# Kernel optimization log

Measured on AMD Instinct MI355X. Metric: run time of the kernel, lower is better.

Reference implementation:

```python
import jax, jax.numpy as jnp
import numpy as np

B, T, IN, CELL, OUT = 512, 32, 512, 128, 128


def setup_inputs() -> dict:
    key = jax.random.key(0)
    ks = jax.random.split(key, 6)
    d = IN + CELL
    w = lambda k, shape, fan: jax.random.normal(k, shape, jnp.float32) / np.sqrt(fan).astype(np.float32)
    return {
        "x": jax.random.normal(ks[0], (B, T, IN), jnp.float32),
        "Wf": w(ks[1], (d, CELL), d), "bf": jnp.zeros((CELL,), jnp.float32),
        "Wi1": w(ks[2], (d, CELL), d), "bi1": jnp.zeros((CELL,), jnp.float32),
        "Wi2": w(ks[3], (d, CELL), d), "bi2": jnp.zeros((CELL,), jnp.float32),
        "Wo": w(ks[4], (d, CELL), d), "bo": jnp.zeros((CELL,), jnp.float32),
        "Wc": w(ks[5], (CELL, OUT), CELL), "bc": jnp.zeros((OUT,), jnp.float32),
    }


def reference(x, Wf, bf, Wi1, bi1, Wi2, bi2, Wo, bo, Wc, bc):
    # Faithful to MyLSTM.forward: loop runs x.shape[1] times; each iteration
    # concatenates the FULL [B,T,CELL] cell_state with the FULL [B,T,IN] x
    # (x is never sliced per step). Only the last iteration's output matters,
    # but we carry it through the scan to match the loop structure exactly.
    Tn = x.shape[1]
    c0 = jnp.zeros(x.shape[:2] + (Wf.shape[1],), x.dtype)
    out0 = jnp.zeros(x.shape[:2] + (Wc.shape[1],), x.dtype)

    def step(carry, _):
        c, _prev_out = carry
        inp = jnp.concatenate([c, x], axis=-1)  # [B,T,CELL+IN]
        f = jax.nn.sigmoid(inp @ Wf + bf)
        c = c * f + jax.nn.sigmoid(inp @ Wi1 + bi1) * jnp.tanh(inp @ Wi2 + bi2)
        o = jax.nn.sigmoid(inp @ Wo + bo) * jnp.tanh(c)
        out = jax.nn.softmax(o @ Wc + bc, axis=2)  # out_features != 1 branch
        return (c, out), None

    (c, out), _ = jax.lax.scan(step, (c0, out0), None, length=Tn)
    return out, c
```

## Files before the change

kernel.cpp:

```cpp
#include <hip/hip_runtime.h>
#include <stdint.h>

#define ROWS  16384
#define CELL  128
#define INF   512
#define RPB   32
#define NSTEP 32

#define LOG2E 1.4426950408889634f

typedef _Float16 f16x8 __attribute__((ext_vector_type(8)));
typedef _Float16 f16x4 __attribute__((ext_vector_type(4)));
typedef float    f32x16 __attribute__((ext_vector_type(16)));

#define MFMA32(a, b, c) __builtin_amdgcn_mfma_f32_32x32x16_f16((a), (b), (c), 0, 0, 0)

#if __has_builtin(__builtin_amdgcn_exp2f)
#define EXP2(x) __builtin_amdgcn_exp2f(x)
#else
#define EXP2(x) __expf((x) * 0.6931471805599453f)
#endif
#define RCP(x) __builtin_amdgcn_rcpf(x)

#define XOFF  65536
#define WCOFF 327680
#define WSTOT 344064

__device__ __forceinline__ unsigned short f2h_bits(float f) {
  _Float16 h = (_Float16)f;
  return *(unsigned short*)&h;
}

__global__ __launch_bounds__(256) void prep_kernel(
    const float* __restrict__ Wf, const float* __restrict__ Wi1,
    const float* __restrict__ Wi2, const float* __restrict__ Wo,
    const float* __restrict__ Wc, unsigned short* __restrict__ ws) {
  int id = blockIdx.x * blockDim.x + threadIdx.x;
  if (id >= WSTOT) return;
  const float* Wg[4] = {Wf, Wi1, Wi2, Wo};
  const float sc[4] = {-LOG2E, -LOG2E, 2.f * LOG2E, -LOG2E};
  if (id < XOFF) {
    int g = id >> 14, r = id & 16383;
    int w = r >> 12, ks = (r >> 9) & 7, lane = (r >> 3) & 63, j = r & 7;
    int k = ks * 16 + ((lane >> 5) << 3) + j;
    int n = w * 32 + (lane & 31);
    ws[id] = f2h_bits(Wg[g][k * CELL + n] * sc[g]);
  } else if (id < WCOFF) {
    int t = id - XOFF;
    int g = t >> 16, r = t & 65535;
    int w = r >> 14, ks = (r >> 9) & 31, lane = (r >> 3) & 63, j = r & 7;
    int k = ks * 16 + ((lane >> 5) << 3) + j;
    int n = w * 32 + (lane & 31);
    ws[id] = f2h_bits(Wg[g][(CELL + k) * CELL + n] * sc[g]);
  } else {
    int r = id - WCOFF;
    int w = r >> 12, ks = (r >> 9) & 7, lane = (r >> 3) & 63, j = r & 7;
    int k = ks * 16 + ((lane >> 5) << 3) + j;
    int n = w * 32 + (lane & 31);
    ws[id] = f2h_bits(Wc[k * CELL + n] * LOG2E);
  }
}

__global__ __launch_bounds__(256, 2) void lstm_kernel(
    const float* __restrict__ x,
    const float* __restrict__ bf_, const float* __restrict__ bi1,
    const float* __restrict__ bi2, const float* __restrict__ bo,
    const float* __restrict__ bc,
    const unsigned short* __restrict__ ws, float* __restrict__ out) {

  __shared__ union {
    _Float16 xs[32][264];
    struct {
      _Float16 o[32][136];
      float    s[32][132];
    } ep;
  } uS;
  __shared__ _Float16 cT[2][32][136];

  const int tid  = threadIdx.x;
  const int lane = tid & 63;
  const int w    = tid >> 6;
  const int n31  = lane & 31;
  const int l5   = lane >> 5;
  const int r0   = blockIdx.x * RPB;

  const _Float16* Aw  = (const _Float16*)ws;
  const _Float16* Xw  = (const _Float16*)ws + XOFF;
  const _Float16* Wcw = (const _Float16*)ws + WCOFF;

  f32x16 u[4];
#pragma unroll
  for (int g = 0; g < 4; ++g)
#pragma unroll
    for (int i = 0; i < 16; ++i) u[g][i] = 0.f;

  const float* xbase = x + (size_t)r0 * INF;
#pragma unroll 1
  for (int ch = 0; ch < 2; ++ch) {
    if (ch) __syncthreads();
#pragma unroll
    for (int i = 0; i < 8; ++i) {
      int flat = tid + i * 256;
      int row = flat >> 6, c4 = flat & 63;
      const float4 v = ((const float4*)(xbase + (size_t)row * INF + ch * 256))[c4];
      f16x4 h = {(_Float16)v.x, (_Float16)v.y, (_Float16)v.z, (_Float16)v.w};
      *(f16x4*)&uS.xs[row][c4 * 4] = h;
    }
    __syncthreads();
#pragma unroll 2
    for (int ksl = 0; ksl < 16; ++ksl) {
      f16x8 b = *(const f16x8*)&uS.xs[n31][ksl * 16 + l5 * 8];
      int ks = ch * 16 + ksl;
#pragma unroll
      for (int g = 0; g < 4; ++g) {
        f16x8 a = *(const f16x8*)(Xw + (((g * 4 + w) * 32 + ks) * 64 + lane) * 8);
        u[g] = MFMA32(a, b, u[g]);
      }
    }
  }
#pragma unroll
  for (int reg = 0; reg < 16; ++reg) {
    int col = w * 32 + (reg & 3) + 8 * (reg >> 2) + 4 * l5;
    u[0][reg] += bf_[col] * (-LOG2E);
    u[1][reg] += bi1[col] * (-LOG2E);
    u[2][reg] += bi2[col] * (2.f * LOG2E);
    u[3][reg] += bo[col]  * (-LOG2E);
  }

  f16x8 wr[3][8];
#pragma unroll
  for (int g = 0; g < 3; ++g)
#pragma unroll
    for (int ks = 0; ks < 8; ++ks)
      wr[g][ks] = *(const f16x8*)(Aw + (((g * 4 + w) * 8 + ks) * 64 + lane) * 8);

  f32x16 cr;
#pragma unroll
  for (int reg = 0; reg < 16; ++reg) {
    float ig = RCP(1.f + EXP2(u[1][reg]));
    float gg = fmaf(-2.f, RCP(1.f + EXP2(u[2][reg])), 1.f);
    cr[reg] = ig * gg;
  }
#pragma unroll
  for (int qd = 0; qd < 4; ++qd) {
    f16x4 p = {(_Float16)cr[qd * 4 + 0], (_Float16)cr[qd * 4 + 1],
               (_Float16)cr[qd * 4 + 2], (_Float16)cr[qd * 4 + 3]};
    *(f16x4*)&cT[0][n31][w * 32 + qd * 8 + l5 * 4] = p;
  }
  __syncthreads();

#pragma unroll 1
  for (int t = 1; t < NSTEP - 1; ++t) {
    const int rb = (t + 1) & 1, wb = t & 1;
    f16x8 b[8];
#pragma unroll
    for (int ks = 0; ks < 8; ++ks)
      b[ks] = *(const f16x8*)&cT[rb][n31][ks * 16 + l5 * 8];
    f32x16 zf = u[0], zi1 = u[1], zi2 = u[2];
#pragma unroll
    for (int ks = 0; ks < 8; ++ks) {
      zf  = MFMA32(wr[0][ks], b[ks], zf);
      zi1 = MFMA32(wr[1][ks], b[ks], zi1);
      zi2 = MFMA32(wr[2][ks], b[ks], zi2);
    }
#pragma unroll
    for (int reg = 0; reg < 16; ++reg) {
      float fg = RCP(1.f + EXP2(zf[reg]));
      float ig = RCP(1.f + EXP2(zi1[reg]));
      float gg = fmaf(-2.f, RCP(1.f + EXP2(zi2[reg])), 1.f);
      cr[reg] = fmaf(cr[reg], fg, ig * gg);
    }
#pragma unroll
    for (int qd = 0; qd < 4; ++qd) {
      f16x4 p = {(_Float16)cr[qd * 4 + 0], (_Float16)cr[qd * 4 + 1],
                 (_Float16)cr[qd * 4 + 2], (_Float16)cr[qd * 4 + 3]};
      *(f16x4*)&cT[wb][n31][w * 32 + qd * 8 + l5 * 4] = p;
    }
    __syncthreads();
  }

  {
    f16x8 b[8];
#pragma unroll
    for (int ks = 0; ks < 8; ++ks)
      b[ks] = *(const f16x8*)&cT[0][n31][ks * 16 + l5 * 8];
    f32x16 zf = u[0], zi1 = u[1], zi2 = u[2], zo = u[3];
#pragma unroll
    for (int ks = 0; ks < 8; ++ks) {
      f16x8 wof = *(const f16x8*)(Aw + (((3 * 4 + w) * 8 + ks) * 64 + lane) * 8);
      zf  = MFMA32(wr[0][ks], b[ks], zf);
      zi1 = MFMA32(wr[1][ks], b[ks], zi1);
      zi2 = MFMA32(wr[2][ks], b[ks], zi2);
      zo  = MFMA32(wof, b[ks], zo);
    }
    float ovv[16];
#pragma unroll
    for (int reg = 0; reg < 16; ++reg) {
      float fg = RCP(1.f + EXP2(zf[reg]));
      float ig = RCP(1.f + EXP2(zi1[reg]));
      float gg = fmaf(-2.f, RCP(1.f + EXP2(zi2[reg])), 1.f);
      float cn = fmaf(cr[reg], fg, ig * gg);
      cr[reg] = cn;
      float th = fmaf(-2.f, RCP(1.f + EXP2(cn * (2.f * LOG2E))), 1.f);
      ovv[reg] = RCP(1.f + EXP2(zo[reg])) * th;
    }
#pragma unroll
    for (int qd = 0; qd < 4; ++qd) {
      f16x4 p = {(_Float16)ovv[qd * 4 + 0], (_Float16)ovv[qd * 4 + 1],
                 (_Float16)ovv[qd * 4 + 2], (_Float16)ovv[qd * 4 + 3]};
      *(f16x4*)&uS.ep.o[n31][w * 32 + qd * 8 + l5 * 4] = p;
    }
    __syncthreads();
  }

  {
    f32x16 sa;
#pragma unroll
    for (int i = 0; i < 16; ++i) sa[i] = 0.f;
#pragma unroll
    for (int ks = 0; ks < 8; ++ks) {
      f16x8 a = *(const f16x8*)(Wcw + ((w * 8 + ks) * 64 + lane) * 8);
      f16x8 b = *(const f16x8*)&uS.ep.o[n31][ks * 16 + l5 * 8];
      sa = MFMA32(a, b, sa);
    }
#pragma unroll
    for (int reg = 0; reg < 16; ++reg) {
      int col = w * 32 + (reg & 3) + 8 * (reg >> 2) + 4 * l5;
      sa[reg] += bc[col] * LOG2E;
    }
#pragma unroll
    for (int qd = 0; qd < 4; ++qd) {
      float4 p = {sa[qd * 4 + 0], sa[qd * 4 + 1], sa[qd * 4 + 2], sa[qd * 4 + 3]};
      *(float4*)&uS.ep.s[n31][w * 32 + qd * 8 + l5 * 4] = p;
    }
    __syncthreads();

#pragma unroll
    for (int rr = 0; rr < 8; ++rr) {
      int r = w * 8 + rr;
      float v0 = uS.ep.s[r][lane];
      float v1 = uS.ep.s[r][lane + 64];
      float m = fmaxf(v0, v1);
#pragma unroll
      for (int off = 32; off; off >>= 1) m = fmaxf(m, __shfl_xor(m, off, 64));
      float e0 = EXP2(v0 - m), e1 = EXP2(v1 - m);
      float sm = e0 + e1;
#pragma unroll
      for (int off = 32; off; off >>= 1) sm += __shfl_xor(sm, off, 64);
      float inv = RCP(sm);
      size_t base = (size_t)(r0 + r) * 128;
      out[base + lane]      = e0 * inv;
      out[base + lane + 64] = e1 * inv;
    }

#pragma unroll
    for (int qd = 0; qd < 4; ++qd) {
      float4 p = {cr[qd * 4 + 0], cr[qd * 4 + 1], cr[qd * 4 + 2], cr[qd * 4 + 3]};
      *(float4*)&out[(size_t)ROWS * 128 + (size_t)(r0 + n31) * 128 +
                     w * 32 + qd * 8 + l5 * 4] = p;
    }
  }
}

extern "C" void kernel_launch(void* const* d_in, const int* in_sizes, int n_in,
                              void* d_out, int out_size, void* d_ws, size_t ws_size,
                              hipStream_t stream) {
  const float* x   = (const float*)d_in[0];
  const float* Wf  = (const float*)d_in[1];
  const float* bf_ = (const float*)d_in[2];
  const float* Wi1 = (const float*)d_in[3];
  const float* bi1 = (const float*)d_in[4];
  const float* Wi2 = (const float*)d_in[5];
  const float* bi2 = (const float*)d_in[6];
  const float* Wo  = (const float*)d_in[7];
  const float* bo  = (const float*)d_in[8];
  const float* Wc  = (const float*)d_in[9];
  const float* bc  = (const float*)d_in[10];
  unsigned short* ws = (unsigned short*)d_ws;
  float* out = (float*)d_out;

  hipLaunchKernelGGL(prep_kernel, dim3((WSTOT + 255) / 256), dim3(256), 0, stream,
                     Wf, Wi1, Wi2, Wo, Wc, ws);
  hipLaunchKernelGGL(lstm_kernel, dim3(ROWS / RPB), dim3(256), 0, stream,
                     x, bf_, bi1, bi2, bo, bc, ws, out);
}
```

Before: 178.9 us.

## Process 64 rows per block with two MFMA row groups and swizzled cell LDS

Each block now handles 64 rows as two 32-row groups, so every wave's register-resident recurrent weights feed twice as many MFMAs and the per-step barrier cost is spread over more work. The output-gate input projection moves to shared memory to free registers. The cell-state LDS layout becomes an XOR-swizzled buffer to avoid bank conflicts. In exchange, occupancy drops to one block per CU, the grid is halved (256 blocks), and register pressure rises with the doubled accumulators.

```diff
diff --git a/kernel.cpp b/kernel.cpp
--- a/kernel.cpp
+++ b/kernel.cpp
@@ -4,7 +4,7 @@
 #define ROWS  16384
 #define CELL  128
 #define INF   512
-#define RPB   32
+#define RPB   64
 #define NSTEP 32
 
 #define LOG2E 1.4426950408889634f
@@ -61,7 +61,7 @@
   }
 }
 
-__global__ __launch_bounds__(256, 2) void lstm_kernel(
+__global__ __launch_bounds__(256, 1) void lstm_kernel(
     const float* __restrict__ x,
     const float* __restrict__ bf_, const float* __restrict__ bi1,
     const float* __restrict__ bi2, const float* __restrict__ bo,
@@ -69,37 +69,41 @@
     const unsigned short* __restrict__ ws, float* __restrict__ out) {
 
   __shared__ union {
-    _Float16 xs[32][264];
+    _Float16 xs[64][268];
     struct {
-      _Float16 o[32][136];
-      float    s[32][132];
+      _Float16 o[64][136];
+      float    s[64][132];
     } ep;
   } uS;
-  __shared__ _Float16 cT[2][32][136];
+  __shared__ _Float16 cT[2][2][32][128];
+  __shared__ float    uo[2][128][33];
 
   const int tid  = threadIdx.x;
   const int lane = tid & 63;
   const int w    = tid >> 6;
   const int n31  = lane & 31;
   const int l5   = lane >> 5;
+  const int key  = (n31 & 15) << 1;
   const int r0   = blockIdx.x * RPB;
 
   const _Float16* Aw  = (const _Float16*)ws;
   const _Float16* Xw  = (const _Float16*)ws + XOFF;
   const _Float16* Wcw = (const _Float16*)ws + WCOFF;
 
-  f32x16 u[4];
+  f32x16 u[4][2];
 #pragma unroll
   for (int g = 0; g < 4; ++g)
 #pragma unroll
-    for (int i = 0; i < 16; ++i) u[g][i] = 0.f;
+    for (int gr = 0; gr < 2; ++gr)
+#pragma unroll
+      for (int i = 0; i < 16; ++i) u[g][gr][i] = 0.f;
 
   const float* xbase = x + (size_t)r0 * INF;
 #pragma unroll 1
   for (int ch = 0; ch < 2; ++ch) {
     if (ch) __syncthreads();
 #pragma unroll
-    for (int i = 0; i < 8; ++i) {
+    for (int i = 0; i < 16; ++i) {
       int flat = tid + i * 256;
       int row = flat >> 6, c4 = flat & 63;
       const float4 v = ((const float4*)(xbase + (size_t)row * INF + ch * 256))[c4];
@@ -109,22 +113,29 @@
     __syncthreads();
 #pragma unroll 2
     for (int ksl = 0; ksl < 16; ++ksl) {
-      f16x8 b = *(const f16x8*)&uS.xs[n31][ksl * 16 + l5 * 8];
+      f16x8 b0 = *(const f16x8*)&uS.xs[n31][ksl * 16 + l5 * 8];
+      f16x8 b1 = *(const f16x8*)&uS.xs[32 + n31][ksl * 16 + l5 * 8];
       int ks = ch * 16 + ksl;
 #pragma unroll
       for (int g = 0; g < 4; ++g) {
         f16x8 a = *(const f16x8*)(Xw + (((g * 4 + w) * 32 + ks) * 64 + lane) * 8);
-        u[g] = MFMA32(a, b, u[g]);
+        u[g][0] = MFMA32(a, b0, u[g][0]);
+        u[g][1] = MFMA32(a, b1, u[g][1]);
       }
     }
   }
 #pragma unroll
   for (int reg = 0; reg < 16; ++reg) {
     int col = w * 32 + (reg & 3) + 8 * (reg >> 2) + 4 * l5;
-    u[0][reg] += bf_[col] * (-LOG2E);
-    u[1][reg] += bi1[col] * (-LOG2E);
-    u[2][reg] += bi2[col] * (2.f * LOG2E);
-    u[3][reg] += bo[col]  * (-LOG2E);
+    float b0v = bf_[col] * (-LOG2E);
+    float b1v = bi1[col] * (-LOG2E);
+    float b2v = bi2[col] * (2.f * LOG2E);
+    float b3v = bo[col]  * (-LOG2E);
+    u[0][0][reg] += b0v; u[0][1][reg] += b0v;
+    u[1][0][reg] += b1v; u[1][1][reg] += b1v;
+    u[2][0][reg] += b2v; u[2][1][reg] += b2v;
+    uo[0][col][n31] = u[3][0][reg] + b3v;
+    uo[1][col][n31] = u[3][1][reg] + b3v;
   }
 
   f16x8 wr[3][8];
@@ -134,110 +145,169 @@
     for (int ks = 0; ks < 8; ++ks)
       wr[g][ks] = *(const f16x8*)(Aw + (((g * 4 + w) * 8 + ks) * 64 + lane) * 8);
 
-  f32x16 cr;
-#pragma unroll
-  for (int reg = 0; reg < 16; ++reg) {
-    float ig = RCP(1.f + EXP2(u[1][reg]));
-    float gg = fmaf(-2.f, RCP(1.f + EXP2(u[2][reg])), 1.f);
-    cr[reg] = ig * gg;
-  }
-#pragma unroll
-  for (int qd = 0; qd < 4; ++qd) {
-    f16x4 p = {(_Float16)cr[qd * 4 + 0], (_Float16)cr[qd * 4 + 1],
-               (_Float16)cr[qd * 4 + 2], (_Float16)cr[qd * 4 + 3]};
-    *(f16x4*)&cT[0][n31][w * 32 + qd * 8 + l5 * 4] = p;
+  f32x16 cr[2];
+#pragma unroll
+  for (int gr = 0; gr < 2; ++gr) {
+#pragma unroll
+    for (int reg = 0; reg < 16; ++reg) {
+      float ig = RCP(1.f + EXP2(u[1][gr][reg]));
+      float gg = fmaf(-2.f, RCP(1.f + EXP2(u[2][gr][reg])), 1.f);
+      cr[gr][reg] = ig * gg;
+    }
+#pragma unroll
+    for (int qd = 0; qd < 4; ++qd) {
+      f16x4 p = {(_Float16)cr[gr][qd * 4 + 0], (_Float16)cr[gr][qd * 4 + 1],
+                 (_Float16)cr[gr][qd * 4 + 2], (_Float16)cr[gr][qd * 4 + 3]};
+      int pos = (w * 8 + qd * 2 + l5) ^ key;
+      *(f16x4*)&cT[0][gr][n31][pos * 4] = p;
+    }
   }
   __syncthreads();
 
 #pragma unroll 1
   for (int t = 1; t < NSTEP - 1; ++t) {
     const int rb = (t + 1) & 1, wb = t & 1;
-    f16x8 b[8];
-#pragma unroll
-    for (int ks = 0; ks < 8; ++ks)
-      b[ks] = *(const f16x8*)&cT[rb][n31][ks * 16 + l5 * 8];
-    f32x16 zf = u[0], zi1 = u[1], zi2 = u[2];
-#pragma unroll
-    for (int ks = 0; ks < 8; ++ks) {
-      zf  = MFMA32(wr[0][ks], b[ks], zf);
-      zi1 = MFMA32(wr[1][ks], b[ks], zi1);
-      zi2 = MFMA32(wr[2][ks], b[ks], zi2);
+    f16x8 b0[8], b1[8];
+#pragma unroll
+    for (int ks = 0; ks < 8; ++ks) {
+      int pos = (ks * 4 + l5 * 2) ^ key;
+      b0[ks] = *(const f16x8*)&cT[rb][0][n31][pos * 4];
+      b1[ks] = *(const f16x8*)&cT[rb][1][n31][pos * 4];
+    }
+    f32x16 zf0 = u[0][0], zi10 = u[1][0], zi20 = u[2][0];
+    f32x16 zf1 = u[0][1], zi11 = u[1][1], zi21 = u[2][1];
+#pragma unroll
+    for (int ks = 0; ks < 8; ++ks) {
+      zf0  = MFMA32(wr[0][ks], b0[ks], zf0);
+      zi10 = MFMA32(wr[1][ks], b0[ks], zi10);
+      zi20 = MFMA32(wr[2][ks], b0[ks], zi20);
+    }
+#pragma unroll
+    for (int ks = 0; ks < 8; ++ks) {
+      zf1  = MFMA32(wr[0][ks], b1[ks], zf1);
+      zi11 = MFMA32(wr[1][ks], b1[ks], zi11);
+      zi21 = MFMA32(wr[2][ks], b1[ks], zi21);
     }
 #pragma unroll
     for (int reg = 0; reg < 16; ++reg) {
-      float fg = RCP(1.f + EXP2(zf[reg]));
-      float ig = RCP(1.f + EXP2(zi1[reg]));
-      float gg = fmaf(-2.f, RCP(1.f + EXP2(zi2[reg])), 1.f);
-      cr[reg] = fmaf(cr[reg], fg, ig * gg);
+      float fg = RCP(1.f + EXP2(zf0[reg]));
+      float ig = RCP(1.f + EXP2(zi10[reg]));
+      float gg = fmaf(-2.f, RCP(1.f + EXP2(zi20[reg])), 1.f);
+      cr[0][reg] = fmaf(cr[0][reg], fg, ig * gg);
     }
 #pragma unroll
     for (int qd = 0; qd < 4; ++qd) {
-      f16x4 p = {(_Float16)cr[qd * 4 + 0], (_Float16)cr[qd * 4 + 1],
-                 (_Float16)cr[qd * 4 + 2], (_Float16)cr[qd * 4 + 3]};
-      *(f16x4*)&cT[wb][n31][w * 32 + qd * 8 + l5 * 4] = p;
+      f16x4 p = {(_Float16)cr[0][qd * 4 + 0], (_Float16)cr[0][qd * 4 + 1],
+                 (_Float16)cr[0][qd * 4 + 2], (_Float16)cr[0][qd * 4 + 3]};
+      int pos = (w * 8 + qd * 2 + l5) ^ key;
+      *(f16x4*)&cT[wb][0][n31][pos * 4] = p;
+    }
+#pragma unroll
+    for (int reg = 0; reg < 16; ++reg) {
+      float fg = RCP(1.f + EXP2(zf1[reg]));
+      float ig = RCP(1.f + EXP2(zi11[reg]));
+      float gg = fmaf(-2.f, RCP(1.f + EXP2(zi21[reg])), 1.f);
+      cr[1][reg] = fmaf(cr[1][reg], fg, ig * gg);
+    }
+#pragma unroll
+    for (int qd = 0; qd < 4; ++qd) {
+      f16x4 p = {(_Float16)cr[1][qd * 4 + 0], (_Float16)cr[1][qd * 4 + 1],
+                 (_Float16)cr[1][qd * 4 + 2], (_Float16)cr[1][qd * 4 + 3]};
+      int pos = (w * 8 + qd * 2 + l5) ^ key;
+      *(f16x4*)&cT[wb][1][n31][pos * 4] = p;
     }
     __syncthreads();
   }
 
   {
-    f16x8 b[8];
-#pragma unroll
-    for (int ks = 0; ks < 8; ++ks)
-      b[ks] = *(const f16x8*)&cT[0][n31][ks * 16 + l5 * 8];
-    f32x16 zf = u[0], zi1 = u[1], zi2 = u[2], zo = u[3];
-#pragma unroll
-    for (int ks = 0; ks < 8; ++ks) {
-      f16x8 wof = *(const f16x8*)(Aw + (((3 * 4 + w) * 8 + ks) * 64 + lane) * 8);
-      zf  = MFMA32(wr[0][ks], b[ks], zf);
-      zi1 = MFMA32(wr[1][ks], b[ks], zi1);
-      zi2 = MFMA32(wr[2][ks], b[ks], zi2);
-      zo  = MFMA32(wof, b[ks], zo);
-    }
-    float ovv[16];
-#pragma unroll
-    for (int reg = 0; reg < 16; ++reg) {
-      float fg = RCP(1.f + EXP2(zf[reg]));
-      float ig = RCP(1.f + EXP2(zi1[reg]));
-      float gg = fmaf(-2.f, RCP(1.f + EXP2(zi2[reg])), 1.f);
-      float cn = fmaf(cr[reg], fg, ig * gg);
-      cr[reg] = cn;
-      float th = fmaf(-2.f, RCP(1.f + EXP2(cn * (2.f * LOG2E))), 1.f);
-      ovv[reg] = RCP(1.f + EXP2(zo[reg])) * th;
-    }
-#pragma unroll
-    for (int qd = 0; qd < 4; ++qd) {
-      f16x4 p = {(_Float16)ovv[qd * 4 + 0], (_Float16)ovv[qd * 4 + 1],
-                 (_Float16)ovv[qd * 4 + 2], (_Float16)ovv[qd * 4 + 3]};
-      *(f16x4*)&uS.ep.o[n31][w * 32 + qd * 8 + l5 * 4] = p;
-    }
-    __syncthreads();
-  }
-
-  {
-    f32x16 sa;
-#pragma unroll
-    for (int i = 0; i < 16; ++i) sa[i] = 0.f;
-#pragma unroll
-    for (int ks = 0; ks < 8; ++ks) {
-      f16x8 a = *(const f16x8*)(Wcw + ((w * 8 + ks) * 64 + lane) * 8);
-      f16x8 b = *(const f16x8*)&uS.ep.o[n31][ks * 16 + l5 * 8];
-      sa = MFMA32(a, b, sa);
-    }
+    f16x8 b0[8], b1[8];
+#pragma unroll
+    for (int ks = 0; ks < 8; ++ks) {
+      int pos = (ks * 4 + l5 * 2) ^ key;
+      b0[ks] = *(const f16x8*)&cT[0][0][n31][pos * 4];
+      b1[ks] = *(const f16x8*)&cT[0][1][n31][pos * 4];
+    }
+    f32x16 zf0 = u[0][0], zi10 = u[1][0], zi20 = u[2][0], zo0;
+    f32x16 zf1 = u[0][1], zi11 = u[1][1], zi21 = u[2][1], zo1;
 #pragma unroll
     for (int reg = 0; reg < 16; ++reg) {
       int col = w * 32 + (reg & 3) + 8 * (reg >> 2) + 4 * l5;
-      sa[reg] += bc[col] * LOG2E;
-    }
-#pragma unroll
-    for (int qd = 0; qd < 4; ++qd) {
-      float4 p = {sa[qd * 4 + 0], sa[qd * 4 + 1], sa[qd * 4 + 2], sa[qd * 4 + 3]};
-      *(float4*)&uS.ep.s[n31][w * 32 + qd * 8 + l5 * 4] = p;
-    }
-    __syncthreads();
-
-#pragma unroll
-    for (int rr = 0; rr < 8; ++rr) {
-      int r = w * 8 + rr;
+      zo0[reg] = uo[0][col][n31];
+      zo1[reg] = uo[1][col][n31];
+    }
+#pragma unroll
+    for (int ks = 0; ks < 8; ++ks) {
+      f16x8 wof = *(const f16x8*)(Aw + (((3 * 4 + w) * 8 + ks) * 64 + lane) * 8);
+      zf0  = MFMA32(wr[0][ks], b0[ks], zf0);
+      zi10 = MFMA32(wr[1][ks], b0[ks], zi10);
+      zi20 = MFMA32(wr[2][ks], b0[ks], zi20);
+      zo0  = MFMA32(wof, b0[ks], zo0);
+      zf1  = MFMA32(wr[0][ks], b1[ks], zf1);
+      zi11 = MFMA32(wr[1][ks], b1[ks], zi11);
+      zi21 = MFMA32(wr[2][ks], b1[ks], zi21);
+      zo1  = MFMA32(wof, b1[ks], zo1);
+    }
+    __syncthreads();
+#pragma unroll
+    for (int gr = 0; gr < 2; ++gr) {
+      const f32x16& zf  = gr ? zf1 : zf0;
+      const f32x16& zi1 = gr ? zi11 : zi10;
+      const f32x16& zi2 = gr ? zi21 : zi20;
+      const f32x16& zo  = gr ? zo1 : zo0;
+      float ovv[16];
+#pragma unroll
+      for (int reg = 0; reg < 16; ++reg) {
+        float fg = RCP(1.f + EXP2(zf[reg]));
+        float ig = RCP(1.f + EXP2(zi1[reg]));
+        float gg = fmaf(-2.f, RCP(1.f + EXP2(zi2[reg])), 1.f);
+        float cn = fmaf(cr[gr][reg], fg, ig * gg);
+        cr[gr][reg] = cn;
+        float th = fmaf(-2.f, RCP(1.f + EXP2(cn * (2.f * LOG2E))), 1.f);
+        ovv[reg] = RCP(1.f + EXP2(zo[reg])) * th;
+      }
+#pragma unroll
+      for (int qd = 0; qd < 4; ++qd) {
+        f16x4 p = {(_Float16)ovv[qd * 4 + 0], (_Float16)ovv[qd * 4 + 1],
+                   (_Float16)ovv[qd * 4 + 2], (_Float16)ovv[qd * 4 + 3]};
+        *(f16x4*)&uS.ep.o[gr * 32 + n31][w * 32 + qd * 8 + l5 * 4] = p;
+      }
+    }
+    __syncthreads();
+  }
+
+  {
+    f32x16 sa[2];
+#pragma unroll
+    for (int gr = 0; gr < 2; ++gr)
+#pragma unroll
+      for (int i = 0; i < 16; ++i) sa[gr][i] = 0.f;
+#pragma unroll
+    for (int ks = 0; ks < 8; ++ks) {
+      f16x8 a  = *(const f16x8*)(Wcw + ((w * 8 + ks) * 64 + lane) * 8);
+      f16x8 p0 = *(const f16x8*)&uS.ep.o[n31][ks * 16 + l5 * 8];
+      f16x8 p1 = *(const f16x8*)&uS.ep.o[32 + n31][ks * 16 + l5 * 8];
+      sa[0] = MFMA32(a, p0, sa[0]);
+      sa[1] = MFMA32(a, p1, sa[1]);
+    }
+#pragma unroll
+    for (int gr = 0; gr < 2; ++gr) {
+#pragma unroll
+      for (int reg = 0; reg < 16; ++reg) {
+        int col = w * 32 + (reg & 3) + 8 * (reg >> 2) + 4 * l5;
+        sa[gr][reg] += bc[col] * LOG2E;
+      }
+#pragma unroll
+      for (int qd = 0; qd < 4; ++qd) {
+        float4 p = {sa[gr][qd * 4 + 0], sa[gr][qd * 4 + 1],
+                    sa[gr][qd * 4 + 2], sa[gr][qd * 4 + 3]};
+        *(float4*)&uS.ep.s[gr * 32 + n31][w * 32 + qd * 8 + l5 * 4] = p;
+      }
+    }
+    __syncthreads();
+
+#pragma unroll
+    for (int rr = 0; rr < 16; ++rr) {
+      int r = w * 16 + rr;
       float v0 = uS.ep.s[r][lane];
       float v1 = uS.ep.s[r][lane + 64];
       float m = fmaxf(v0, v1);
@@ -254,11 +324,14 @@
     }
 
 #pragma unroll
-    for (int qd = 0; qd < 4; ++qd) {
-      float4 p = {cr[qd * 4 + 0], cr[qd * 4 + 1], cr[qd * 4 + 2], cr[qd * 4 + 3]};
-      *(float4*)&out[(size_t)ROWS * 128 + (size_t)(r0 + n31) * 128 +
-                     w * 32 + qd * 8 + l5 * 4] = p;
-    }
+    for (int gr = 0; gr < 2; ++gr)
+#pragma unroll
+      for (int qd = 0; qd < 4; ++qd) {
+        float4 p = {cr[gr][qd * 4 + 0], cr[gr][qd * 4 + 1],
+                    cr[gr][qd * 4 + 2], cr[gr][qd * 4 + 3]};
+        *(float4*)&out[(size_t)ROWS * 128 + (size_t)(r0 + gr * 32 + n31) * 128 +
+                       w * 32 + qd * 8 + l5 * 4] = p;
+      }
   }
 }
 
```

Result: slower. 185.8 us (+3.8%).

## Restructure LSTM kernel so each wave owns 16 rows with 16x16 MFMA, no block barriers

Applied to the files above, without the earlier changes.

The recurrence is re-partitioned so that each wave owns 16 full rows and all 128 cell columns, using 16x16x32 MFMA tiles. The per-step cross-wave __syncthreads goes away because each wave only reads back its own cell state from a swizzled LDS buffer. Gate preactivations from x are stored in LDS as fp16, biases are pre-scaled in the prep kernel, and gate math is merged into a single reciprocal. Rows per block double to 64 at one block per CU, which raises register pressure (the recurrent weights are held in registers) and lowers the number of resident blocks. It also loses precision because the x contribution is kept in fp16.

```diff
diff --git a/kernel.cpp b/kernel.cpp
--- a/kernel.cpp
+++ b/kernel.cpp
@@ -4,16 +4,15 @@
 #define ROWS  16384
 #define CELL  128
 #define INF   512
-#define RPB   32
+#define RPB   64
 #define NSTEP 32
-
 #define LOG2E 1.4426950408889634f
 
 typedef _Float16 f16x8 __attribute__((ext_vector_type(8)));
 typedef _Float16 f16x4 __attribute__((ext_vector_type(4)));
-typedef float    f32x16 __attribute__((ext_vector_type(16)));
-
-#define MFMA32(a, b, c) __builtin_amdgcn_mfma_f32_32x32x16_f16((a), (b), (c), 0, 0, 0)
+typedef float    f32x4 __attribute__((ext_vector_type(4)));
+
+#define MFMA16(a, b, c) __builtin_amdgcn_mfma_f32_16x16x32_f16((a), (b), (c), 0, 0, 0)
 
 #if __has_builtin(__builtin_amdgcn_exp2f)
 #define EXP2(x) __builtin_amdgcn_exp2f(x)
@@ -22,9 +21,10 @@
 #endif
 #define RCP(x) __builtin_amdgcn_rcpf(x)
 
-#define XOFF  65536
+#define XWOFF 65536
 #define WCOFF 327680
-#define WSTOT 344064
+#define BOFF  344064
+#define PREPN 344704
 
 __device__ __forceinline__ unsigned short f2h_bits(float f) {
   _Float16 h = (_Float16)f;
@@ -34,230 +34,268 @@
 __global__ __launch_bounds__(256) void prep_kernel(
     const float* __restrict__ Wf, const float* __restrict__ Wi1,
     const float* __restrict__ Wi2, const float* __restrict__ Wo,
-    const float* __restrict__ Wc, unsigned short* __restrict__ ws) {
+    const float* __restrict__ Wc,
+    const float* __restrict__ bf_, const float* __restrict__ bi1,
+    const float* __restrict__ bi2, const float* __restrict__ bo,
+    const float* __restrict__ bc, unsigned short* __restrict__ ws) {
   int id = blockIdx.x * blockDim.x + threadIdx.x;
-  if (id >= WSTOT) return;
+  if (id >= PREPN) return;
   const float* Wg[4] = {Wf, Wi1, Wi2, Wo};
   const float sc[4] = {-LOG2E, -LOG2E, 2.f * LOG2E, -LOG2E};
-  if (id < XOFF) {
-    int g = id >> 14, r = id & 16383;
-    int w = r >> 12, ks = (r >> 9) & 7, lane = (r >> 3) & 63, j = r & 7;
-    int k = ks * 16 + ((lane >> 5) << 3) + j;
-    int n = w * 32 + (lane & 31);
-    ws[id] = f2h_bits(Wg[g][k * CELL + n] * sc[g]);
+  if (id < XWOFF) {
+    int j = id & 7, lane = (id >> 3) & 63, kt = (id >> 9) & 3,
+        mt = (id >> 11) & 7, g = id >> 14;
+    int cin = kt * 32 + ((lane >> 4) << 3) + j;
+    int cout = mt * 16 + (lane & 15);
+    ws[id] = f2h_bits(Wg[g][cin * CELL + cout] * sc[g]);
   } else if (id < WCOFF) {
-    int t = id - XOFF;
-    int g = t >> 16, r = t & 65535;
-    int w = r >> 14, ks = (r >> 9) & 31, lane = (r >> 3) & 63, j = r & 7;
-    int k = ks * 16 + ((lane >> 5) << 3) + j;
-    int n = w * 32 + (lane & 31);
-    ws[id] = f2h_bits(Wg[g][(CELL + k) * CELL + n] * sc[g]);
+    int t = id - XWOFF;
+    int j = t & 7, lane = (t >> 3) & 63, kt = (t >> 9) & 15,
+        mt = (t >> 13) & 7, g = t >> 16;
+    int xf = kt * 32 + ((lane >> 4) << 3) + j;
+    int cout = mt * 16 + (lane & 15);
+    ws[id] = f2h_bits(Wg[g][(CELL + xf) * CELL + cout] * sc[g]);
+  } else if (id < BOFF) {
+    int r = id - WCOFF;
+    int j = r & 7, lane = (r >> 3) & 63, kt = (r >> 9) & 3, mt = (r >> 11) & 7;
+    int cin = kt * 32 + ((lane >> 4) << 3) + j;
+    int cout = mt * 16 + (lane & 15);
+    ws[id] = f2h_bits(Wc[cin * CELL + cout] * LOG2E);
   } else {
-    int r = id - WCOFF;
-    int w = r >> 12, ks = (r >> 9) & 7, lane = (r >> 3) & 63, j = r & 7;
-    int k = ks * 16 + ((lane >> 5) << 3) + j;
-    int n = w * 32 + (lane & 31);
-    ws[id] = f2h_bits(Wc[k * CELL + n] * LOG2E);
+    int i = id - BOFF;
+    int g = i >> 7, cell = i & 127;
+    float v;
+    if (g == 0) v = bf_[cell] * (-LOG2E);
+    else if (g == 1) v = bi1[cell] * (-LOG2E);
+    else if (g == 2) v = bi2[cell] * (2.f * LOG2E);
+    else if (g == 3) v = bo[cell] * (-LOG2E);
+    else v = bc[cell] * LOG2E;
+    ((float*)(ws + BOFF))[i] = v;
   }
 }
 
-__global__ __launch_bounds__(256, 2) void lstm_kernel(
+__global__ __launch_bounds__(256, 1) void lstm_kernel(
     const float* __restrict__ x,
-    const float* __restrict__ bf_, const float* __restrict__ bi1,
-    const float* __restrict__ bi2, const float* __restrict__ bo,
-    const float* __restrict__ bc,
     const unsigned short* __restrict__ ws, float* __restrict__ out) {
 
   __shared__ union {
-    _Float16 xs[32][264];
-    struct {
-      _Float16 o[32][136];
-      float    s[32][132];
-    } ep;
+    _Float16 xs[64 * 512];
+    _Float16 u4[4 * 4 * 8 * 64 * 4];
   } uS;
-  __shared__ _Float16 cT[2][32][136];
+  __shared__ _Float16 cbuf[4 * 2 * 16 * 128];
 
   const int tid  = threadIdx.x;
   const int lane = tid & 63;
-  const int w    = tid >> 6;
-  const int n31  = lane & 31;
-  const int l5   = lane >> 5;
+  const int wv   = tid >> 6;
+  const int n16  = lane & 15;
+  const int q    = lane >> 4;
   const int r0   = blockIdx.x * RPB;
-
-  const _Float16* Aw  = (const _Float16*)ws;
-  const _Float16* Xw  = (const _Float16*)ws + XOFF;
-  const _Float16* Wcw = (const _Float16*)ws + WCOFF;
-
-  f32x16 u[4];
+  const int myrow = wv * 16 + n16;
+
+  const _Float16* W = (const _Float16*)ws;
+  const float* biasf = (const float*)(ws + BOFF);
+
+#pragma unroll
+  for (int i = 0; i < 16; ++i) {
+    int flat = tid + i * 256;
+    int row = flat >> 6, g = flat & 63;
+    int gs = g ^ (row & 15);
+    const float* src = x + (size_t)(r0 + row) * INF + g * 8;
+    float4 v0 = *(const float4*)src;
+    float4 v1 = *(const float4*)(src + 4);
+    f16x8 h = {(_Float16)v0.x, (_Float16)v0.y, (_Float16)v0.z, (_Float16)v0.w,
+               (_Float16)v1.x, (_Float16)v1.y, (_Float16)v1.z, (_Float16)v1.w};
+    *(f16x8*)&uS.xs[row * 512 + gs * 8] = h;
+  }
+  __syncthreads();
+
+  f32x4 acc[4][8];
 #pragma unroll
   for (int g = 0; g < 4; ++g)
 #pragma unroll
-    for (int i = 0; i < 16; ++i) u[g][i] = 0.f;
-
-  const float* xbase = x + (size_t)r0 * INF;
+    for (int mt = 0; mt < 8; ++mt) acc[g][mt] = (f32x4){0.f, 0.f, 0.f, 0.f};
+
+  {
+    const int xbase = myrow * 512;
 #pragma unroll 1
-  for (int ch = 0; ch < 2; ++ch) {
-    if (ch) __syncthreads();
-#pragma unroll
-    for (int i = 0; i < 8; ++i) {
-      int flat = tid + i * 256;
-      int row = flat >> 6, c4 = flat & 63;
-      const float4 v = ((const float4*)(xbase + (size_t)row * INF + ch * 256))[c4];
-      f16x4 h = {(_Float16)v.x, (_Float16)v.y, (_Float16)v.z, (_Float16)v.w};
-      *(f16x4*)&uS.xs[row][c4 * 4] = h;
-    }
-    __syncthreads();
-#pragma unroll 2
-    for (int ksl = 0; ksl < 16; ++ksl) {
-      f16x8 b = *(const f16x8*)&uS.xs[n31][ksl * 16 + l5 * 8];
-      int ks = ch * 16 + ksl;
-#pragma unroll
-      for (int g = 0; g < 4; ++g) {
-        f16x8 a = *(const f16x8*)(Xw + (((g * 4 + w) * 32 + ks) * 64 + lane) * 8);
-        u[g] = MFMA32(a, b, u[g]);
-      }
-    }
-  }
-#pragma unroll
-  for (int reg = 0; reg < 16; ++reg) {
-    int col = w * 32 + (reg & 3) + 8 * (reg >> 2) + 4 * l5;
-    u[0][reg] += bf_[col] * (-LOG2E);
-    u[1][reg] += bi1[col] * (-LOG2E);
-    u[2][reg] += bi2[col] * (2.f * LOG2E);
-    u[3][reg] += bo[col]  * (-LOG2E);
-  }
-
-  f16x8 wr[3][8];
+    for (int kt = 0; kt < 16; ++kt) {
+      f16x8 b = *(const f16x8*)&uS.xs[xbase + (((kt * 4 + q) ^ n16) << 3)];
+#pragma unroll
+      for (int g = 0; g < 4; ++g)
+#pragma unroll
+        for (int mt = 0; mt < 8; ++mt) {
+          f16x8 a = *(const f16x8*)&W[XWOFF + (((g * 8 + mt) * 16 + kt) << 9) + lane * 8];
+          acc[g][mt] = MFMA16(a, b, acc[g][mt]);
+        }
+    }
+  }
+  __syncthreads();
+
+#pragma unroll
+  for (int g = 0; g < 4; ++g)
+#pragma unroll
+    for (int mt = 0; mt < 8; ++mt) {
+      float4 bv = *(const float4*)(biasf + g * 128 + mt * 16 + q * 4);
+      acc[g][mt][0] += bv.x; acc[g][mt][1] += bv.y;
+      acc[g][mt][2] += bv.z; acc[g][mt][3] += bv.w;
+      f16x4 h = {(_Float16)acc[g][mt][0], (_Float16)acc[g][mt][1],
+                 (_Float16)acc[g][mt][2], (_Float16)acc[g][mt][3]};
+      *(f16x4*)&uS.u4[(((wv * 4 + g) * 8 + mt) << 8) + lane * 4] = h;
+    }
+
+  const int cb = wv * 4096 + n16 * 128;
+  int rdo[4], wro[8];
+#pragma unroll
+  for (int kt = 0; kt < 4; ++kt) rdo[kt] = cb + (((kt * 4 + q) ^ n16) << 3);
+#pragma unroll
+  for (int mt = 0; mt < 8; ++mt)
+    wro[mt] = cb + (((mt * 2 + (q >> 1)) ^ n16) << 3) + (q & 1) * 4;
+
+  f32x4 cr[8];
+#pragma unroll
+  for (int mt = 0; mt < 8; ++mt) {
+#pragma unroll
+    for (int r = 0; r < 4; ++r) {
+      float ei = EXP2(fminf(acc[1][mt][r], 30.f));
+      float eg = EXP2(fminf(acc[2][mt][r], 30.f));
+      cr[mt][r] = (eg - 1.f) * RCP((1.f + ei) * (1.f + eg));
+    }
+    f16x4 h = {(_Float16)cr[mt][0], (_Float16)cr[mt][1],
+               (_Float16)cr[mt][2], (_Float16)cr[mt][3]};
+    *(f16x4*)&cbuf[wro[mt]] = h;
+  }
+#if __has_builtin(__builtin_amdgcn_sched_barrier)
+  __builtin_amdgcn_sched_barrier(0);
+#endif
+
+  f16x8 wr[3][8][4];
 #pragma unroll
   for (int g = 0; g < 3; ++g)
 #pragma unroll
-    for (int ks = 0; ks < 8; ++ks)
-      wr[g][ks] = *(const f16x8*)(Aw + (((g * 4 + w) * 8 + ks) * 64 + lane) * 8);
-
-  f32x16 cr;
-#pragma unroll
-  for (int reg = 0; reg < 16; ++reg) {
-    float ig = RCP(1.f + EXP2(u[1][reg]));
-    float gg = fmaf(-2.f, RCP(1.f + EXP2(u[2][reg])), 1.f);
-    cr[reg] = ig * gg;
-  }
-#pragma unroll
-  for (int qd = 0; qd < 4; ++qd) {
-    f16x4 p = {(_Float16)cr[qd * 4 + 0], (_Float16)cr[qd * 4 + 1],
-               (_Float16)cr[qd * 4 + 2], (_Float16)cr[qd * 4 + 3]};
-    *(f16x4*)&cT[0][n31][w * 32 + qd * 8 + l5 * 4] = p;
-  }
-  __syncthreads();
+    for (int mt = 0; mt < 8; ++mt)
+#pragma unroll
+      for (int kt = 0; kt < 4; ++kt)
+        wr[g][mt][kt] = *(const f16x8*)&W[(((g * 8 + mt) * 4 + kt) << 9) + lane * 8];
+
+  const int ub = (wv * 4) * 2048;
 
 #pragma unroll 1
   for (int t = 1; t < NSTEP - 1; ++t) {
-    const int rb = (t + 1) & 1, wb = t & 1;
-    f16x8 b[8];
-#pragma unroll
-    for (int ks = 0; ks < 8; ++ks)
-      b[ks] = *(const f16x8*)&cT[rb][n31][ks * 16 + l5 * 8];
-    f32x16 zf = u[0], zi1 = u[1], zi2 = u[2];
-#pragma unroll
-    for (int ks = 0; ks < 8; ++ks) {
-      zf  = MFMA32(wr[0][ks], b[ks], zf);
-      zi1 = MFMA32(wr[1][ks], b[ks], zi1);
-      zi2 = MFMA32(wr[2][ks], b[ks], zi2);
-    }
-#pragma unroll
-    for (int reg = 0; reg < 16; ++reg) {
-      float fg = RCP(1.f + EXP2(zf[reg]));
-      float ig = RCP(1.f + EXP2(zi1[reg]));
-      float gg = fmaf(-2.f, RCP(1.f + EXP2(zi2[reg])), 1.f);
-      cr[reg] = fmaf(cr[reg], fg, ig * gg);
-    }
-#pragma unroll
-    for (int qd = 0; qd < 4; ++qd) {
-      f16x4 p = {(_Float16)cr[qd * 4 + 0], (_Float16)cr[qd * 4 + 1],
-                 (_Float16)cr[qd * 4 + 2], (_Float16)cr[qd * 4 + 3]};
-      *(f16x4*)&cT[wb][n31][w * 32 + qd * 8 + l5 * 4] = p;
-    }
-    __syncthreads();
+    const int rb = ((t + 1) & 1) * 2048, wb = (t & 1) * 2048;
+    f16x8 b[4];
+#pragma unroll
+    for (int kt = 0; kt < 4; ++kt) b[kt] = *(const f16x8*)&cbuf[rdo[kt] + rb];
+#pragma unroll
+    for (int mt = 0; mt < 8; ++mt) {
+      f16x4 u0 = *(const f16x4*)&uS.u4[ub + (mt << 8) + lane * 4];
+      f16x4 u1 = *(const f16x4*)&uS.u4[ub + 2048 + (mt << 8) + lane * 4];
+      f16x4 u2 = *(const f16x4*)&uS.u4[ub + 4096 + (mt << 8) + lane * 4];
+      f32x4 zf  = {(float)u0[0], (float)u0[1], (float)u0[2], (float)u0[3]};
+      f32x4 zi1 = {(float)u1[0], (float)u1[1], (float)u1[2], (float)u1[3]};
+      f32x4 zi2 = {(float)u2[0], (float)u2[1], (float)u2[2], (float)u2[3]};
+#pragma unroll
+      for (int kt = 0; kt < 4; ++kt) {
+        zf  = MFMA16(wr[0][mt][kt], b[kt], zf);
+        zi1 = MFMA16(wr[1][mt][kt], b[kt], zi1);
+        zi2 = MFMA16(wr[2][mt][kt], b[kt], zi2);
+      }
+#pragma unroll
+      for (int r = 0; r < 4; ++r) {
+        float ef = EXP2(fminf(zf[r],  30.f));
+        float ei = EXP2(fminf(zi1[r], 30.f));
+        float eg = EXP2(fminf(zi2[r], 30.f));
+        float fp1 = 1.f + ef;
+        float p   = (1.f + ei) * (1.f + eg);
+        cr[mt][r] = fmaf(cr[mt][r], p, fp1 * (eg - 1.f)) * RCP(fp1 * p);
+      }
+      f16x4 h = {(_Float16)cr[mt][0], (_Float16)cr[mt][1],
+                 (_Float16)cr[mt][2], (_Float16)cr[mt][3]};
+      *(f16x4*)&cbuf[wro[mt] + wb] = h;
+    }
   }
 
   {
-    f16x8 b[8];
-#pragma unroll
-    for (int ks = 0; ks < 8; ++ks)
-      b[ks] = *(const f16x8*)&cT[0][n31][ks * 16 + l5 * 8];
-    f32x16 zf = u[0], zi1 = u[1], zi2 = u[2], zo = u[3];
-#pragma unroll
-    for (int ks = 0; ks < 8; ++ks) {
-      f16x8 wof = *(const f16x8*)(Aw + (((3 * 4 + w) * 8 + ks) * 64 + lane) * 8);
-      zf  = MFMA32(wr[0][ks], b[ks], zf);
-      zi1 = MFMA32(wr[1][ks], b[ks], zi1);
-      zi2 = MFMA32(wr[2][ks], b[ks], zi2);
-      zo  = MFMA32(wof, b[ks], zo);
-    }
-    float ovv[16];
-#pragma unroll
-    for (int reg = 0; reg < 16; ++reg) {
-      float fg = RCP(1.f + EXP2(zf[reg]));
-      float ig = RCP(1.f + EXP2(zi1[reg]));
-      float gg = fmaf(-2.f, RCP(1.f + EXP2(zi2[reg])), 1.f);
-      float cn = fmaf(cr[reg], fg, ig * gg);
-      cr[reg] = cn;
-      float th = fmaf(-2.f, RCP(1.f + EXP2(cn * (2.f * LOG2E))), 1.f);
-      ovv[reg] = RCP(1.f + EXP2(zo[reg])) * th;
-    }
-#pragma unroll
-    for (int qd = 0; qd < 4; ++qd) {
-      f16x4 p = {(_Float16)ovv[qd * 4 + 0], (_Float16)ovv[qd * 4 + 1],
-                 (_Float16)ovv[qd * 4 + 2], (_Float16)ovv[qd * 4 + 3]};
-      *(f16x4*)&uS.ep.o[n31][w * 32 + qd * 8 + l5 * 4] = p;
-    }
-    __syncthreads();
+    f16x8 b[4];
+#pragma unroll
+    for (int kt = 0; kt < 4; ++kt) b[kt] = *(const f16x8*)&cbuf[rdo[kt]];
+#pragma unroll
+    for (int mt = 0; mt < 8; ++mt) {
+      f16x4 u0 = *(const f16x4*)&uS.u4[ub + (mt << 8) + lane * 4];
+      f16x4 u1 = *(const f16x4*)&uS.u4[ub + 2048 + (mt << 8) + lane * 4];
+      f16x4 u2 = *(const f16x4*)&uS.u4[ub + 4096 + (mt << 8) + lane * 4];
+      f16x4 u3 = *(const f16x4*)&uS.u4[ub + 6144 + (mt << 8) + lane * 4];
+      f32x4 zf  = {(float)u0[0], (float)u0[1], (float)u0[2], (float)u0[3]};
+      f32x4 zi1 = {(float)u1[0], (float)u1[1], (float)u1[2], (float)u1[3]};
+      f32x4 zi2 = {(float)u2[0], (float)u2[1], (float)u2[2], (float)u2[3]};
+      f32x4 zo  = {(float)u3[0], (float)u3[1], (float)u3[2], (float)u3[3]};
+#pragma unroll
+      for (int kt = 0; kt < 4; ++kt) {
+        f16x8 wof = *(const f16x8*)&W[(((3 * 8 + mt) * 4 + kt) << 9) + lane * 8];
+        zf  = MFMA16(wr[0][mt][kt], b[kt], zf);
+        zi1 = MFMA16(wr[1][mt][kt], b[kt], zi1);
+        zi2 = MFMA16(wr[2][mt][kt], b[kt], zi2);
+        zo  = MFMA16(wof, b[kt], zo);
+      }
+      f16x4 h;
+#pragma unroll
+      for (int r = 0; r < 4; ++r) {
+        float ef = EXP2(fminf(zf[r],  30.f));
+        float ei = EXP2(fminf(zi1[r], 30.f));
+        float eg = EXP2(fminf(zi2[r], 30.f));
+        float fp1 = 1.f + ef;
+        float p   = (1.f + ei) * (1.f + eg);
+        float cn  = fmaf(cr[mt][r], p, fp1 * (eg - 1.f)) * RCP(fp1 * p);
+        cr[mt][r] = cn;
+        float eo = EXP2(fminf(zo[r], 30.f));
+        float ec = EXP2(fminf(cn * (2.f * LOG2E), 30.f));
+        h[r] = (_Float16)((ec - 1.f) * RCP((1.f + eo) * (1.f + ec)));
+      }
+      *(f16x4*)&cbuf[wro[mt] + 2048] = h;
+    }
   }
 
   {
-    f32x16 sa;
-#pragma unroll
-    for (int i = 0; i < 16; ++i) sa[i] = 0.f;
-#pragma unroll
-    for (int ks = 0; ks < 8; ++ks) {
-      f16x8 a = *(const f16x8*)(Wcw + ((w * 8 + ks) * 64 + lane) * 8);
-      f16x8 b = *(const f16x8*)&uS.ep.o[n31][ks * 16 + l5 * 8];
-      sa = MFMA32(a, b, sa);
-    }
-#pragma unroll
-    for (int reg = 0; reg < 16; ++reg) {
-      int col = w * 32 + (reg & 3) + 8 * (reg >> 2) + 4 * l5;
-      sa[reg] += bc[col] * LOG2E;
-    }
-#pragma unroll
-    for (int qd = 0; qd < 4; ++qd) {
-      float4 p = {sa[qd * 4 + 0], sa[qd * 4 + 1], sa[qd * 4 + 2], sa[qd * 4 + 3]};
-      *(float4*)&uS.ep.s[n31][w * 32 + qd * 8 + l5 * 4] = p;
-    }
-    __syncthreads();
-
-#pragma unroll
-    for (int rr = 0; rr < 8; ++rr) {
-      int r = w * 8 + rr;
-      float v0 = uS.ep.s[r][lane];
-      float v1 = uS.ep.s[r][lane + 64];
-      float m = fmaxf(v0, v1);
-#pragma unroll
-      for (int off = 32; off; off >>= 1) m = fmaxf(m, __shfl_xor(m, off, 64));
-      float e0 = EXP2(v0 - m), e1 = EXP2(v1 - m);
-      float sm = e0 + e1;
-#pragma unroll
-      for (int off = 32; off; off >>= 1) sm += __shfl_xor(sm, off, 64);
-      float inv = RCP(sm);
-      size_t base = (size_t)(r0 + r) * 128;
-      out[base + lane]      = e0 * inv;
-      out[base + lane + 64] = e1 * inv;
-    }
-
-#pragma unroll
-    for (int qd = 0; qd < 4; ++qd) {
-      float4 p = {cr[qd * 4 + 0], cr[qd * 4 + 1], cr[qd * 4 + 2], cr[qd * 4 + 3]};
-      *(float4*)&out[(size_t)ROWS * 128 + (size_t)(r0 + n31) * 128 +
-                     w * 32 + qd * 8 + l5 * 4] = p;
+    f16x8 ob[4];
+#pragma unroll
+    for (int kt = 0; kt < 4; ++kt) ob[kt] = *(const f16x8*)&cbuf[rdo[kt] + 2048];
+    f32x4 sa[8];
+#pragma unroll
+    for (int mt = 0; mt < 8; ++mt) {
+      float4 bv = *(const float4*)(biasf + 4 * 128 + mt * 16 + q * 4);
+      sa[mt] = (f32x4){bv.x, bv.y, bv.z, bv.w};
+#pragma unroll
+      for (int kt = 0; kt < 4; ++kt) {
+        f16x8 a = *(const f16x8*)&W[WCOFF + ((mt * 4 + kt) << 9) + lane * 8];
+        sa[mt] = MFMA16(a, ob[kt], sa[mt]);
+      }
+    }
+    float m = -1e30f;
+#pragma unroll
+    for (int mt = 0; mt < 8; ++mt)
+#pragma unroll
+      for (int r = 0; r < 4; ++r) m = fmaxf(m, sa[mt][r]);
+    m = fmaxf(m, __shfl_xor(m, 16, 64));
+    m = fmaxf(m, __shfl_xor(m, 32, 64));
+    float sm = 0.f;
+    float ev[8][4];
+#pragma unroll
+    for (int mt = 0; mt < 8; ++mt)
+#pragma unroll
+      for (int r = 0; r < 4; ++r) { ev[mt][r] = EXP2(sa[mt][r] - m); sm += ev[mt][r]; }
+    sm += __shfl_xor(sm, 16, 64);
+    sm += __shfl_xor(sm, 32, 64);
+    float inv = RCP(sm);
+
+    size_t obase = (size_t)(r0 + myrow) * 128;
+#pragma unroll
+    for (int mt = 0; mt < 8; ++mt) {
+      float4 p = {ev[mt][0] * inv, ev[mt][1] * inv, ev[mt][2] * inv, ev[mt][3] * inv};
+      *(float4*)&out[obase + mt * 16 + q * 4] = p;
+    }
+#pragma unroll
+    for (int mt = 0; mt < 8; ++mt) {
+      float4 p = {cr[mt][0], cr[mt][1], cr[mt][2], cr[mt][3]};
+      *(float4*)&out[(size_t)ROWS * 128 + obase + mt * 16 + q * 4] = p;
     }
   }
 }
@@ -279,8 +317,8 @@
   unsigned short* ws = (unsigned short*)d_ws;
   float* out = (float*)d_out;
 
-  hipLaunchKernelGGL(prep_kernel, dim3((WSTOT + 255) / 256), dim3(256), 0, stream,
-                     Wf, Wi1, Wi2, Wo, Wc, ws);
+  hipLaunchKernelGGL(prep_kernel, dim3((PREPN + 255) / 256), dim3(256), 0, stream,
+                     Wf, Wi1, Wi2, Wo, Wc, bf_, bi1, bi2, bo, bc, ws);
   hipLaunchKernelGGL(lstm_kernel, dim3(ROWS / RPB), dim3(256), 0, stream,
-                     x, bf_, bi1, bi2, bo, bc, ws, out);
+                     x, ws, out);
 }
```

Result: slower. 264.9 us (+48.1%).
